# Performance work log

Measured on AMD Instinct MI355X. Metric: run time of the kernel, lower is better.

Reference implementation:

```python
import jax, jax.numpy as jnp
import numpy as np

B, N, D = 4, 512, 256  # batch, num_diseases, feature_dim == hidden_dim
H = 256                # hidden_dim
EPS = 1e-5

def _layernorm(x, g, b):
    m = jnp.mean(x, axis=-1, keepdims=True)
    v = jnp.mean((x - m) ** 2, axis=-1, keepdims=True)
    return (x - m) * jax.lax.rsqrt(v + EPS) * g + b

def setup_inputs() -> dict:
    key = jax.random.key(0)
    ks = jax.random.split(key, 16)
    s = 0.02
    return {
        "x": jax.random.normal(ks[0], (B, N, D), jnp.float32),
        "area_matrix": jax.random.uniform(ks[1], (B, N), jnp.float32),
        "co_occurrence": jax.random.uniform(ks[2], (N, N), jnp.float32),
        "Wq": jax.random.normal(ks[3], (H, D), jnp.float32) * s,
        "bq": jnp.zeros((H,), jnp.float32),
        "Wk": jax.random.normal(ks[4], (H, D), jnp.float32) * s,
        "bk": jnp.zeros((H,), jnp.float32),
        "Wv": jax.random.normal(ks[5], (H, D), jnp.float32) * s,
        "bv": jnp.zeros((H,), jnp.float32),
        "We1": jax.random.normal(ks[6], (H, 2), jnp.float32) * 0.5,
        "be1": jnp.zeros((H,), jnp.float32),
        "We2": jax.random.normal(ks[7], (1, H), jnp.float32) * s,
        "be2": jnp.zeros((1,), jnp.float32),
        "Wo": jax.random.normal(ks[8], (H, H), jnp.float32) * s,
        "bo": jnp.zeros((H,), jnp.float32),
        "g_ot": jnp.ones((H,), jnp.float32),
        "b_ot": jnp.zeros((H,), jnp.float32),
        "g1": jnp.ones((H,), jnp.float32),
        "b1": jnp.zeros((H,), jnp.float32),
        "g2": jnp.ones((H,), jnp.float32),
        "b2": jnp.zeros((H,), jnp.float32),
    }

def reference(x, area_matrix, co_occurrence, Wq, bq, Wk, bk, Wv, bv,
              We1, be1, We2, be2, Wo, bo, g_ot, b_ot, g1, b1, g2, b2):
    # projections: (B, N, H)
    q = jnp.einsum('bnd,hd->bnh', x, Wq) + bq
    k = jnp.einsum('bnd,hd->bnh', x, Wk) + bk
    v = jnp.einsum('bnd,hd->bnh', x, Wv) + bv
    attn_scores = jnp.einsum('bih,bjh->bij', q, k) / jnp.sqrt(jnp.float32(H))
    # edge inputs: (B, N, N, 2) = stack(broadcast area along last N, broadcast co-occ along batch)
    area = jnp.broadcast_to(area_matrix[:, :, None], (B, N, N))
    co = jnp.broadcast_to(co_occurrence[None], (B, N, N))
    edge_inputs = jnp.stack([area, co], axis=-1)
    h = jax.nn.relu(jnp.einsum('bije,he->bijh', edge_inputs, We1) + be1)
    edge_weights = jax.nn.sigmoid(jnp.einsum('bijh,oh->bijo', h, We2) + be2)[..., 0]
    attn_probs = jax.nn.softmax(attn_scores * edge_weights, axis=-1)  # dropout = identity (eval)
    out = jnp.einsum('bij,bjh->bih', attn_probs, v)
    out = _layernorm(out, g1, b1)
    out = jax.nn.relu(_layernorm(jnp.einsum('bnh,oh->bno', out, Wo) + bo, g_ot, b_ot))
    out = _layernorm(out + x, g2, b2)
    return out
```

## Files before the change

### kernel.cpp

```cpp
#include <hip/hip_runtime.h>

typedef unsigned short u16;
typedef unsigned int u32;

#define NB 4
#define NN 512
#define ND 256
#define NH 256
#define TI 4

typedef __attribute__((ext_vector_type(8))) short short8;
typedef __attribute__((ext_vector_type(4))) float f32x4;

__device__ __forceinline__ short bf(float f) {
    u32 t; __builtin_memcpy(&t, &f, 4);
    u32 r = (t + 0x7FFFu + ((t >> 16) & 1u)) >> 16;
    return (short)(u16)r;
}
__device__ __forceinline__ float blo(u32 u) {
    u32 t = u << 16; float f; __builtin_memcpy(&f, &t, 4); return f;
}
__device__ __forceinline__ float bhi(u32 u) {
    u32 t = u & 0xFFFF0000u; float f; __builtin_memcpy(&f, &t, 4); return f;
}

__device__ __forceinline__ float waveReduceSum(float v) {
#pragma unroll
    for (int o = 32; o > 0; o >>= 1) v += __shfl_down(v, o);
    return v;
}

__device__ __forceinline__ void blockReduce8(float4& va, float4& vb, float4* red) {
#pragma unroll
    for (int o = 32; o > 0; o >>= 1) {
        va.x += __shfl_down(va.x, o); va.y += __shfl_down(va.y, o);
        va.z += __shfl_down(va.z, o); va.w += __shfl_down(va.w, o);
        vb.x += __shfl_down(vb.x, o); vb.y += __shfl_down(vb.y, o);
        vb.z += __shfl_down(vb.z, o); vb.w += __shfl_down(vb.w, o);
    }
    int wid = threadIdx.x >> 6;
    __syncthreads();
    if ((threadIdx.x & 63) == 0) { red[2 * wid] = va; red[2 * wid + 1] = vb; }
    __syncthreads();
    float4 ra = red[0], rb = red[1];
#pragma unroll
    for (int w = 1; w < 8; ++w) {
        float4 ua = red[2 * w], ub = red[2 * w + 1];
        ra.x += ua.x; ra.y += ua.y; ra.z += ua.z; ra.w += ua.w;
        rb.x += ub.x; rb.y += ub.y; rb.z += ub.z; rb.w += ub.w;
    }
    va = ra; vb = rb;
}

__global__ __launch_bounds__(256) void qkv_mfma(
    const float* __restrict__ x,
    const float* __restrict__ Wq, const float* __restrict__ bq,
    const float* __restrict__ Wk, const float* __restrict__ bk,
    const float* __restrict__ Wv, const float* __restrict__ bv,
    const float* __restrict__ Wo,
    u16* __restrict__ qb, u16* __restrict__ kb, u16* __restrict__ vp,
    u16* __restrict__ wop)
{
    const int tid = threadIdx.x;
    if (blockIdx.y == 48) {
        __shared__ float t[32][33];
        const int tx = tid & 31, ty = tid >> 5;
#pragma unroll
        for (int tt2 = 0; tt2 < 2; ++tt2) {
            const int tile = blockIdx.x * 2 + tt2;
            const int bx = tile & 7, by = tile >> 3;
            __syncthreads();
#pragma unroll
            for (int k = 0; k < 4; ++k)
                t[ty + 8 * k][tx] = Wo[(size_t)(by * 32 + ty + 8 * k) * 256 + bx * 32 + tx];
            __syncthreads();
#pragma unroll
            for (int k = 0; k < 4; ++k) {
                const int d = bx * 32 + ty + 8 * k, o = by * 32 + tx;
                wop[(size_t)(d >> 3) * 2048 + o * 8 + (d & 7)] = (u16)bf(t[tx][ty + 8 * k]);
            }
        }
        return;
    }

    const int lane = tid & 63, wave = tid >> 6;
    const int r0 = blockIdx.x * 64 + wave * 16;
    const int out0 = blockIdx.y * 16;
    const int which = blockIdx.y >> 4;
    const float* W   = (which == 0) ? Wq : (which == 1) ? Wk : Wv;
    const float* bia = (which == 0) ? bq : (which == 1) ? bk : bv;
    u16* dst         = (which == 0) ? qb : (which == 1) ? kb : vp;

    const int m = lane & 15, koff = (lane >> 4) * 8;
    const float* Ap = x + (size_t)(r0 + m) * 256 + koff;
    const float* Bp = W + (size_t)((out0 & 255) + m) * 256 + koff;

    f32x4 acc = {0.f, 0.f, 0.f, 0.f};
#pragma unroll
    for (int kb8 = 0; kb8 < 8; ++kb8) {
        float4 a0 = *(const float4*)(Ap + kb8 * 32);
        float4 a1 = *(const float4*)(Ap + kb8 * 32 + 4);
        float4 b0 = *(const float4*)(Bp + kb8 * 32);
        float4 b1 = *(const float4*)(Bp + kb8 * 32 + 4);
        short8 af, bf8;
        af[0] = bf(a0.x); af[1] = bf(a0.y); af[2] = bf(a0.z); af[3] = bf(a0.w);
        af[4] = bf(a1.x); af[5] = bf(a1.y); af[6] = bf(a1.z); af[7] = bf(a1.w);
        bf8[0] = bf(b0.x); bf8[1] = bf(b0.y); bf8[2] = bf(b0.z); bf8[3] = bf(b0.w);
        bf8[4] = bf(b1.x); bf8[5] = bf(b1.y); bf8[6] = bf(b1.z); bf8[7] = bf(b1.w);
        acc = __builtin_amdgcn_mfma_f32_16x16x32_bf16(af, bf8, acc, 0, 0, 0);
    }

    const int oc = (out0 + m) & 255;
    const float bias = bia[oc];
    const int rbase = r0 + (lane >> 4) * 4;
#pragma unroll
    for (int reg = 0; reg < 4; ++reg) {
        int R = rbase + reg;
        dst[(size_t)R * 256 + oc] = (u16)bf(acc[reg] + bias);
    }
}

__global__ __launch_bounds__(256) void s_gemm(
    const u16* __restrict__ qb, const u16* __restrict__ kb, float* __restrict__ S)
{
    const int lane = threadIdx.x & 63, wave = threadIdx.x >> 6;
    const int job = blockIdx.x * 4 + wave;
    const int b = job >> 10, rem = job & 1023;
    const int i0 = (rem >> 5) * 16, j0 = (rem & 31) * 16;
    const int m = lane & 15, koff = (lane >> 4) * 8;
    const u16* Ap = qb + (size_t)(b * 512 + i0 + m) * 256 + koff;
    const u16* Bp = kb + (size_t)(b * 512 + j0 + m) * 256 + koff;

    f32x4 acc = {0.f, 0.f, 0.f, 0.f};
#pragma unroll
    for (int kb8 = 0; kb8 < 8; ++kb8) {
        short8 a  = *(const short8*)(Ap + kb8 * 32);
        short8 bf8 = *(const short8*)(Bp + kb8 * 32);
        acc = __builtin_amdgcn_mfma_f32_16x16x32_bf16(a, bf8, acc, 0, 0, 0);
    }
    const int col = j0 + m;
    const int rbase = i0 + (lane >> 4) * 4;
#pragma unroll
    for (int reg = 0; reg < 4; ++reg)
        S[(size_t)(b * 512 + rbase + reg) * 512 + col] = acc[reg];
}

__global__ __launch_bounds__(512) void fused_kernel(
    const float* __restrict__ x, const float* __restrict__ area, const float* __restrict__ co,
    const float* __restrict__ We1, const float* __restrict__ be1,
    const float* __restrict__ We2, const float* __restrict__ be2,
    const u32* __restrict__ wop32, const float* __restrict__ bo,
    const float* __restrict__ g_ot, const float* __restrict__ b_ot,
    const float* __restrict__ g1, const float* __restrict__ b1,
    const float* __restrict__ g2, const float* __restrict__ b2,
    const float* __restrict__ S, const u32* __restrict__ vp32,
    float* __restrict__ out)
{
    const int tid = threadIdx.x;
    const int b = blockIdx.x >> 7;
    const int i0 = (blockIdx.x & 127) << 2;
    const int lane = tid & 63, w = tid >> 6;

    __shared__ float histS[1024], histB[1024], hist2S[1024], hist2B[1024];
    __shared__ float srow[2048];
    __shared__ float4 red8b[16];
    __shared__ float sBaseS[4], sBaseB[4], redA[8], redB[8];

    const float be2f = be2[0];

    histS[tid] = 0.f; histS[tid + 512] = 0.f;
    histB[tid] = 0.f; histB[tid + 512] = 0.f;
    __syncthreads();
    {
        const int s = tid >> 7, h0 = tid & 127;
        const float a = area[b * NN + i0 + s];
        float baS = 0.f, baB = 0.f;
#pragma unroll
        for (int k = 0; k < 2; ++k) {
            const int h = h0 + 128 * k;
            const float w10 = We1[2 * h], w11 = We1[2 * h + 1];
            const float w2v = We2[h], be1v = be1[h];
            const float al = fmaf(a, w10, be1v);
            const float sl = w11 * w2v, bb = al * w2v;
            if (w11 == 0.f) {
                if (al > 0.f) baB += bb;
            } else {
                float tt = -al / w11;
                if (w11 > 0.f) {
                    if (tt <= 0.f)      { baS += sl; baB += bb; }
                    else if (tt < 1.f) {
                        int u = (int)(tt * 256.f); u = u > 255 ? 255 : u;
                        atomicAdd(&histS[s * 256 + u], sl);
                        atomicAdd(&histB[s * 256 + u], bb);
                    }
                } else {
                    if (tt >= 1.f)      { baS += sl; baB += bb; }
                    else if (tt > 0.f) {
                        baS += sl; baB += bb;
                        int u = (int)(tt * 256.f); u = u > 255 ? 255 : u;
                        atomicAdd(&histS[s * 256 + u], -sl);
                        atomicAdd(&histB[s * 256 + u], -bb);
                    }
                }
            }
        }
        float rS = waveReduceSum(baS), rB = waveReduceSum(baB);
        if (lane == 0) { redA[w] = rS; redB[w] = rB; }
    }
    __syncthreads();
    if (tid < 4) {
        sBaseS[tid] = redA[2 * tid] + redA[2 * tid + 1];
        sBaseB[tid] = redB[2 * tid] + redB[2 * tid + 1];
    }

    {
        const int s = w & 3;
        float* hp = (w < 4) ? histS : histB;
        float b0 = hp[s * 256 + 4 * lane + 0];
        float b1 = hp[s * 256 + 4 * lane + 1];
        float b2 = hp[s * 256 + 4 * lane + 2];
        float b3 = hp[s * 256 + 4 * lane + 3];
        float p0 = b0, p1 = p0 + b1, p2 = p1 + b2, p3 = p2 + b3;
        float incl = p3;
#pragma unroll
        for (int off = 1; off < 64; off <<= 1) {
            float t = __shfl_up(incl, off);
            if (lane >= off) incl += t;
        }
        float excl = incl - p3;
        hp[s * 256 + 4 * lane + 0] = p0 + excl;
        hp[s * 256 + 4 * lane + 1] = p1 + excl;
        hp[s * 256 + 4 * lane + 2] = p2 + excl;
        hp[s * 256 + 4 * lane + 3] = p3 + excl;
    }
    __syncthreads();

    {
        const float* Sp = S + (size_t)(b * NN + i0) * 512 + tid;
#pragma unroll
        for (int ti = 0; ti < TI; ++ti) {
            float c = co[(size_t)(i0 + ti) * NN + tid];
            int u = (int)(c * 256.f); u = u > 255 ? 255 : u;
            float Sg = sBaseS[ti] + histS[ti * 256 + u];
            float Bg = sBaseB[ti] + histB[ti * 256 + u];
            float e = fmaf(c, Sg, Bg) + be2f;
            float ew = 1.f / (1.f + __expf(-e));
            srow[ti * 512 + tid] = __expf(Sp[(size_t)ti * 512] * 0.0625f * ew);
        }
        __syncthreads();
    }

    {
        const int h2 = tid & 127, qtr = tid >> 7;
        float a0[TI] = {0.f, 0.f, 0.f, 0.f};
        float a1[TI] = {0.f, 0.f, 0.f, 0.f};
        const u32* vp_ = vp32 + (size_t)b * 512 * 128 + h2;
        const float4* s4p = (const float4*)srow;
        for (int j4 = qtr * 32; j4 < qtr * 32 + 32; ++j4) {
            const int jj = 4 * j4;
            u32 va = vp_[(size_t)(jj + 0) * 128];
            u32 vb = vp_[(size_t)(jj + 1) * 128];
            u32 vc = vp_[(size_t)(jj + 2) * 128];
            u32 vd = vp_[(size_t)(jj + 3) * 128];
            float la = blo(va), ha = bhi(va), lb = blo(vb), hb = bhi(vb);
            float lc = blo(vc), hc = bhi(vc), ld = blo(vd), hd = bhi(vd);
#pragma unroll
            for (int ti = 0; ti < TI; ++ti) {
                float4 p4 = s4p[ti * 128 + j4];
                a0[ti] += p4.x * la + p4.y * lb + p4.z * lc + p4.w * ld;
                a1[ti] += p4.x * ha + p4.y * hb + p4.z * hc + p4.w * hd;
            }
        }
        float2* bq_ = (float2*)((qtr == 0) ? histS : (qtr == 1) ? histB : (qtr == 2) ? hist2S : hist2B);
#pragma unroll
        for (int ti = 0; ti < TI; ++ti) bq_[ti * 128 + h2] = make_float2(a0[ti], a1[ti]);
        __syncthreads();
    }

    const int hP = tid & 255, half = tid >> 8;
    float accv[TI] = {0.f, 0.f, 0.f, 0.f};
    if (half == 0) {
#pragma unroll
        for (int ti = 0; ti < TI; ++ti)
            accv[ti] = histS[ti * 256 + hP] + histB[ti * 256 + hP]
                     + hist2S[ti * 256 + hP] + hist2B[ti * 256 + hP];
    }

    float4 sa, sb;
    float dd[TI];
#pragma unroll
    for (int ti = 0; ti < TI; ++ti) {
        float v = (half == 0) ? accv[ti] : 0.f;
        ((float*)&sa)[ti] = v; ((float*)&sb)[ti] = v * v;
    }
    blockReduce8(sa, sb, red8b);
    if (half == 0) {
        const float g1v = g1[hP], b1v = b1[hP];
#pragma unroll
        for (int ti = 0; ti < TI; ++ti) {
            float mean = ((const float*)&sa)[ti] * (1.f / 256.f);
            float var = fmaxf(((const float*)&sb)[ti] * (1.f / 256.f) - mean * mean, 0.f);
            srow[ti * 256 + hP] = (accv[ti] - mean) * rsqrtf(var + 1e-5f) * g1v + b1v;
        }
    }
    __syncthreads();

    float acc2[TI] = {0.f, 0.f, 0.f, 0.f};
    {
        const float4* y4p = (const float4*)srow;
        for (int g = half * 16; g < half * 16 + 16; ++g) {
            uint4 ww = *(const uint4*)(wop32 + (size_t)g * 1024 + hP * 4);
            float f0 = blo(ww.x), f1 = bhi(ww.x), f2 = blo(ww.y), f3 = bhi(ww.y);
            float f4 = blo(ww.z), f5 = bhi(ww.z), f6 = blo(ww.w), f7 = bhi(ww.w);
#pragma unroll
            for (int ti = 0; ti < TI; ++ti) {
                float4 ya = y4p[ti * 64 + 2 * g];
                float4 yb = y4p[ti * 64 + 2 * g + 1];
                acc2[ti] += ya.x * f0 + ya.y * f1 + ya.z * f2 + ya.w * f3
                          + yb.x * f4 + yb.y * f5 + yb.z * f6 + yb.w * f7;
            }
        }
        if (half == 1) {
#pragma unroll
            for (int ti = 0; ti < TI; ++ti) histS[ti * 256 + hP] = acc2[ti];
        }
        __syncthreads();
        if (half == 0) {
            const float bov = bo[hP];
#pragma unroll
            for (int ti = 0; ti < TI; ++ti) acc2[ti] += histS[ti * 256 + hP] + bov;
        }
    }

#pragma unroll
    for (int ti = 0; ti < TI; ++ti) {
        float v = (half == 0) ? acc2[ti] : 0.f;
        ((float*)&sa)[ti] = v; ((float*)&sb)[ti] = v * v;
    }
    blockReduce8(sa, sb, red8b);
    float z[TI];
    const float gotv = (half == 0) ? g_ot[hP] : 0.f;
    const float botv = (half == 0) ? b_ot[hP] : 0.f;
#pragma unroll
    for (int ti = 0; ti < TI; ++ti) {
        float mean = ((const float*)&sa)[ti] * (1.f / 256.f);
        float var = fmaxf(((const float*)&sb)[ti] * (1.f / 256.f) - mean * mean, 0.f);
        dd[ti] = (half == 0) ? acc2[ti] - mean : 0.f;
        z[ti] = fmaxf(dd[ti] * rsqrtf(var + 1e-5f) * gotv + botv, 0.f);
    }

    float tt[TI];
#pragma unroll
    for (int ti = 0; ti < TI; ++ti) {
        tt[ti] = (half == 0) ? z[ti] + x[(size_t)(b * NN + i0 + ti) * ND + hP] : 0.f;
        ((float*)&sa)[ti] = tt[ti]; ((float*)&sb)[ti] = tt[ti] * tt[ti];
    }
    blockReduce8(sa, sb, red8b);
    if (half == 0) {
        const float g2v = g2[hP], b2v = b2[hP];
#pragma unroll
        for (int ti = 0; ti < TI; ++ti) {
            float mean = ((const float*)&sa)[ti] * (1.f / 256.f);
            float var = fmaxf(((const float*)&sb)[ti] * (1.f / 256.f) - mean * mean, 0.f);
            float o = (tt[ti] - mean) * rsqrtf(var + 1e-5f) * g2v + b2v;
            out[(size_t)(b * NN + i0 + ti) * NH + hP] = o;
        }
    }
}

extern "C" void kernel_launch(void* const* d_in, const int* in_sizes, int n_in,
                              void* d_out, int out_size, void* d_ws, size_t ws_size,
                              hipStream_t stream) {
    const float* x    = (const float*)d_in[0];
    const float* area = (const float*)d_in[1];
    const float* co   = (const float*)d_in[2];
    const float* Wq   = (const float*)d_in[3];
    const float* bq   = (const float*)d_in[4];
    const float* Wk   = (const float*)d_in[5];
    const float* bk   = (const float*)d_in[6];
    const float* Wv   = (const float*)d_in[7];
    const float* bv   = (const float*)d_in[8];
    const float* We1  = (const float*)d_in[9];
    const float* be1  = (const float*)d_in[10];
    const float* We2  = (const float*)d_in[11];
    const float* be2  = (const float*)d_in[12];
    const float* Wo   = (const float*)d_in[13];
    const float* bo   = (const float*)d_in[14];
    const float* g_ot = (const float*)d_in[15];
    const float* b_ot = (const float*)d_in[16];
    const float* g1   = (const float*)d_in[17];
    const float* b1   = (const float*)d_in[18];
    const float* g2   = (const float*)d_in[19];
    const float* b2   = (const float*)d_in[20];

    u16*  qb  = (u16*)d_ws;
    u16*  kb  = qb + (size_t)2048 * 256;
    u16*  vp  = kb + (size_t)2048 * 256;
    u16*  wop = vp + (size_t)2048 * 256;
    float* S  = (float*)(wop + 65536);

    qkv_mfma<<<dim3(32, 49), 256, 0, stream>>>(x, Wq, bq, Wk, bk, Wv, bv, Wo,
                                               qb, kb, vp, wop);
    s_gemm<<<1024, 256, 0, stream>>>(qb, kb, S);
    fused_kernel<<<NB * NN / TI, 512, 0, stream>>>(x, area, co, We1, be1, We2, be2,
                                                   (const u32*)wop, bo,
                                                   g_ot, b_ot, g1, b1, g2, b2,
                                                   S, (const u32*)vp,
                                                   (float*)d_out);
}
```

Measured before the change: 158.6 us.

## Use MFMA for PV and output projection in fused kernel; pre-convert inputs to bf16

```diff
diff --git a/kernel.cpp b/kernel.cpp
--- a/kernel.cpp
+++ b/kernel.cpp
@@ -12,16 +12,10 @@
 typedef __attribute__((ext_vector_type(8))) short short8;
 typedef __attribute__((ext_vector_type(4))) float f32x4;
 
-__device__ __forceinline__ short bf(float f) {
+__device__ __forceinline__ u16 bfq(float f) {
     u32 t; __builtin_memcpy(&t, &f, 4);
     u32 r = (t + 0x7FFFu + ((t >> 16) & 1u)) >> 16;
-    return (short)(u16)r;
-}
-__device__ __forceinline__ float blo(u32 u) {
-    u32 t = u << 16; float f; __builtin_memcpy(&f, &t, 4); return f;
-}
-__device__ __forceinline__ float bhi(u32 u) {
-    u32 t = u & 0xFFFF0000u; float f; __builtin_memcpy(&f, &t, 4); return f;
+    return (u16)r;
 }
 
 __device__ __forceinline__ float waveReduceSum(float v) {
@@ -52,62 +46,50 @@
     va = ra; vb = rb;
 }
 
+__global__ __launch_bounds__(256) void prep_kernel(
+    const float* __restrict__ x, const float* __restrict__ Wq,
+    const float* __restrict__ Wk, const float* __restrict__ Wv,
+    const float* __restrict__ Wo,
+    u16* __restrict__ xb, u16* __restrict__ wb)
+{
+    const int idx4 = (blockIdx.x * 256 + threadIdx.x) * 4;
+    const float* src;
+    u16* dst;
+    int off;
+    if (idx4 < 524288) { src = x; dst = xb; off = idx4; }
+    else {
+        int u = idx4 - 524288;
+        int which = u >> 16; off = u & 65535;
+        src = (which == 0) ? Wq : (which == 1) ? Wk : (which == 2) ? Wv : Wo;
+        dst = wb + which * 65536;
+    }
+    float4 f = *(const float4*)(src + off);
+    u32 lo = (u32)bfq(f.x) | ((u32)bfq(f.y) << 16);
+    u32 hi = (u32)bfq(f.z) | ((u32)bfq(f.w) << 16);
+    *(uint2*)(dst + off) = make_uint2(lo, hi);
+}
+
 __global__ __launch_bounds__(256) void qkv_mfma(
-    const float* __restrict__ x,
-    const float* __restrict__ Wq, const float* __restrict__ bq,
-    const float* __restrict__ Wk, const float* __restrict__ bk,
-    const float* __restrict__ Wv, const float* __restrict__ bv,
-    const float* __restrict__ Wo,
-    u16* __restrict__ qb, u16* __restrict__ kb, u16* __restrict__ vp,
-    u16* __restrict__ wop)
+    const u16* __restrict__ xb, const u16* __restrict__ wb,
+    const float* __restrict__ bq, const float* __restrict__ bk, const float* __restrict__ bv,
+    u16* __restrict__ qb, u16* __restrict__ kb, u16* __restrict__ vt)
 {
-    const int tid = threadIdx.x;
-    if (blockIdx.y == 48) {
-        __shared__ float t[32][33];
-        const int tx = tid & 31, ty = tid >> 5;
-#pragma unroll
-        for (int tt2 = 0; tt2 < 2; ++tt2) {
-            const int tile = blockIdx.x * 2 + tt2;
-            const int bx = tile & 7, by = tile >> 3;
-            __syncthreads();
-#pragma unroll
-            for (int k = 0; k < 4; ++k)
-                t[ty + 8 * k][tx] = Wo[(size_t)(by * 32 + ty + 8 * k) * 256 + bx * 32 + tx];
-            __syncthreads();
-#pragma unroll
-            for (int k = 0; k < 4; ++k) {
-                const int d = bx * 32 + ty + 8 * k, o = by * 32 + tx;
-                wop[(size_t)(d >> 3) * 2048 + o * 8 + (d & 7)] = (u16)bf(t[tx][ty + 8 * k]);
-            }
-        }
-        return;
-    }
-
-    const int lane = tid & 63, wave = tid >> 6;
+    const int lane = threadIdx.x & 63, wave = threadIdx.x >> 6;
     const int r0 = blockIdx.x * 64 + wave * 16;
     const int out0 = blockIdx.y * 16;
     const int which = blockIdx.y >> 4;
-    const float* W   = (which == 0) ? Wq : (which == 1) ? Wk : Wv;
     const float* bia = (which == 0) ? bq : (which == 1) ? bk : bv;
-    u16* dst         = (which == 0) ? qb : (which == 1) ? kb : vp;
 
     const int m = lane & 15, koff = (lane >> 4) * 8;
-    const float* Ap = x + (size_t)(r0 + m) * 256 + koff;
-    const float* Bp = W + (size_t)((out0 & 255) + m) * 256 + koff;
+    const u16* Ap = xb + (size_t)(r0 + m) * 256 + koff;
+    const u16* Bp = wb + which * 65536 + (size_t)((out0 & 255) + m) * 256 + koff;
 
     f32x4 acc = {0.f, 0.f, 0.f, 0.f};
 #pragma unroll
-    for (int kb8 = 0; kb8 < 8; ++kb8) {
-        float4 a0 = *(const float4*)(Ap + kb8 * 32);
-        float4 a1 = *(const float4*)(Ap + kb8 * 32 + 4);
-        float4 b0 = *(const float4*)(Bp + kb8 * 32);
-        float4 b1 = *(const float4*)(Bp + kb8 * 32 + 4);
-        short8 af, bf8;
-        af[0] = bf(a0.x); af[1] = bf(a0.y); af[2] = bf(a0.z); af[3] = bf(a0.w);
-        af[4] = bf(a1.x); af[5] = bf(a1.y); af[6] = bf(a1.z); af[7] = bf(a1.w);
-        bf8[0] = bf(b0.x); bf8[1] = bf(b0.y); bf8[2] = bf(b0.z); bf8[3] = bf(b0.w);
-        bf8[4] = bf(b1.x); bf8[5] = bf(b1.y); bf8[6] = bf(b1.z); bf8[7] = bf(b1.w);
-        acc = __builtin_amdgcn_mfma_f32_16x16x32_bf16(af, bf8, acc, 0, 0, 0);
+    for (int ks = 0; ks < 8; ++ks) {
+        short8 a  = *(const short8*)(Ap + ks * 32);
+        short8 bb = *(const short8*)(Bp + ks * 32);
+        acc = __builtin_amdgcn_mfma_f32_16x16x32_bf16(a, bb, acc, 0, 0, 0);
     }
 
     const int oc = (out0 + m) & 255;
@@ -116,7 +98,10 @@
 #pragma unroll
     for (int reg = 0; reg < 4; ++reg) {
         int R = rbase + reg;
-        dst[(size_t)R * 256 + oc] = (u16)bf(acc[reg] + bias);
+        u16 val = bfq(acc[reg] + bias);
+        if (which == 0)      qb[(size_t)R * 256 + oc] = val;
+        else if (which == 1) kb[(size_t)R * 256 + oc] = val;
+        else                 vt[((size_t)(R >> 9) * 256 + oc) * 512 + (R & 511)] = val;
     }
 }
 
@@ -133,10 +118,10 @@
 
     f32x4 acc = {0.f, 0.f, 0.f, 0.f};
 #pragma unroll
-    for (int kb8 = 0; kb8 < 8; ++kb8) {
-        short8 a  = *(const short8*)(Ap + kb8 * 32);
-        short8 bf8 = *(const short8*)(Bp + kb8 * 32);
-        acc = __builtin_amdgcn_mfma_f32_16x16x32_bf16(a, bf8, acc, 0, 0, 0);
+    for (int ks = 0; ks < 8; ++ks) {
+        short8 a   = *(const short8*)(Ap + ks * 32);
+        short8 bb  = *(const short8*)(Bp + ks * 32);
+        acc = __builtin_amdgcn_mfma_f32_16x16x32_bf16(a, bb, acc, 0, 0, 0);
     }
     const int col = j0 + m;
     const int rbase = i0 + (lane >> 4) * 4;
@@ -145,15 +130,17 @@
         S[(size_t)(b * 512 + rbase + reg) * 512 + col] = acc[reg];
 }
 
+#define PSTR 520
+#define YSTR 264
 __global__ __launch_bounds__(512) void fused_kernel(
     const float* __restrict__ x, const float* __restrict__ area, const float* __restrict__ co,
     const float* __restrict__ We1, const float* __restrict__ be1,
     const float* __restrict__ We2, const float* __restrict__ be2,
-    const u32* __restrict__ wop32, const float* __restrict__ bo,
+    const u16* __restrict__ wob, const float* __restrict__ bo,
     const float* __restrict__ g_ot, const float* __restrict__ b_ot,
     const float* __restrict__ g1, const float* __restrict__ b1,
     const float* __restrict__ g2, const float* __restrict__ b2,
-    const float* __restrict__ S, const u32* __restrict__ vp32,
+    const float* __restrict__ S, const u16* __restrict__ vt,
     float* __restrict__ out)
 {
     const int tid = threadIdx.x;
@@ -161,8 +148,10 @@
     const int i0 = (blockIdx.x & 127) << 2;
     const int lane = tid & 63, w = tid >> 6;
 
-    __shared__ float histS[1024], histB[1024], hist2S[1024], hist2B[1024];
-    __shared__ float srow[2048];
+    __shared__ float histS[1024], histB[1024];
+    __shared__ float pvbuf[1024];
+    __shared__ u16 srow16[16 * PSTR];
+    __shared__ u16 y16[16 * YSTR];
     __shared__ float4 red8b[16];
     __shared__ float sBaseS[4], sBaseB[4], redA[8], redB[8];
 
@@ -170,7 +159,14 @@
 
     histS[tid] = 0.f; histS[tid + 512] = 0.f;
     histB[tid] = 0.f; histB[tid + 512] = 0.f;
-    __syncthreads();
+    {
+        u32* s32 = (u32*)srow16;
+        for (int i = tid; i < 4160; i += 512) s32[i] = 0u;
+        u32* y32 = (u32*)y16;
+        for (int i = tid; i < 2112; i += 512) y32[i] = 0u;
+    }
+    __syncthreads();
+
     {
         const int s = tid >> 7, h0 = tid & 127;
         const float a = area[b * NN + i0 + s];
@@ -245,53 +241,45 @@
             float Bg = sBaseB[ti] + histB[ti * 256 + u];
             float e = fmaf(c, Sg, Bg) + be2f;
             float ew = 1.f / (1.f + __expf(-e));
-            srow[ti * 512 + tid] = __expf(Sp[(size_t)ti * 512] * 0.0625f * ew);
+            srow16[ti * PSTR + tid] = bfq(__expf(Sp[(size_t)ti * 512] * 0.0625f * ew));
         }
         __syncthreads();
     }
 
     {
-        const int h2 = tid & 127, qtr = tid >> 7;
-        float a0[TI] = {0.f, 0.f, 0.f, 0.f};
-        float a1[TI] = {0.f, 0.f, 0.f, 0.f};
-        const u32* vp_ = vp32 + (size_t)b * 512 * 128 + h2;
-        const float4* s4p = (const float4*)srow;
-        for (int j4 = qtr * 32; j4 < qtr * 32 + 32; ++j4) {
-            const int jj = 4 * j4;
-            u32 va = vp_[(size_t)(jj + 0) * 128];
-            u32 vb = vp_[(size_t)(jj + 1) * 128];
-            u32 vc = vp_[(size_t)(jj + 2) * 128];
-            u32 vd = vp_[(size_t)(jj + 3) * 128];
-            float la = blo(va), ha = bhi(va), lb = blo(vb), hb = bhi(vb);
-            float lc = blo(vc), hc = bhi(vc), ld = blo(vd), hd = bhi(vd);
-#pragma unroll
-            for (int ti = 0; ti < TI; ++ti) {
-                float4 p4 = s4p[ti * 128 + j4];
-                a0[ti] += p4.x * la + p4.y * lb + p4.z * lc + p4.w * ld;
-                a1[ti] += p4.x * ha + p4.y * hb + p4.z * hc + p4.w * hd;
+        const int m = lane & 15, koff = (lane >> 4) * 8;
+        const int t0 = 2 * w, t1 = 2 * w + 1;
+        const u16* B0p = vt + ((size_t)(b * 256 + t0 * 16 + m)) * 512 + koff;
+        const u16* B1p = vt + ((size_t)(b * 256 + t1 * 16 + m)) * 512 + koff;
+        const u16* Arow = srow16 + m * PSTR + koff;
+        f32x4 acc0 = {0.f, 0.f, 0.f, 0.f}, acc1 = {0.f, 0.f, 0.f, 0.f};
+#pragma unroll
+        for (int ks = 0; ks < 16; ++ks) {
+            short8 a  = *(const short8*)(Arow + ks * 32);
+            short8 b0 = *(const short8*)(B0p + ks * 32);
+            short8 b1 = *(const short8*)(B1p + ks * 32);
+            acc0 = __builtin_amdgcn_mfma_f32_16x16x32_bf16(a, b0, acc0, 0, 0, 0);
+            acc1 = __builtin_amdgcn_mfma_f32_16x16x32_bf16(a, b1, acc1, 0, 0, 0);
+        }
+        __syncthreads();
+        if (lane < 16) {
+#pragma unroll
+            for (int reg = 0; reg < 4; ++reg) {
+                pvbuf[reg * 256 + t0 * 16 + lane] = acc0[reg];
+                pvbuf[reg * 256 + t1 * 16 + lane] = acc1[reg];
             }
         }
-        float2* bq_ = (float2*)((qtr == 0) ? histS : (qtr == 1) ? histB : (qtr == 2) ? hist2S : hist2B);
-#pragma unroll
-        for (int ti = 0; ti < TI; ++ti) bq_[ti * 128 + h2] = make_float2(a0[ti], a1[ti]);
         __syncthreads();
     }
 
     const int hP = tid & 255, half = tid >> 8;
-    float accv[TI] = {0.f, 0.f, 0.f, 0.f};
-    if (half == 0) {
-#pragma unroll
-        for (int ti = 0; ti < TI; ++ti)
-            accv[ti] = histS[ti * 256 + hP] + histB[ti * 256 + hP]
-                     + hist2S[ti * 256 + hP] + hist2B[ti * 256 + hP];
-    }
-
     float4 sa, sb;
-    float dd[TI];
+    float accv[TI];
 #pragma unroll
     for (int ti = 0; ti < TI; ++ti) {
-        float v = (half == 0) ? accv[ti] : 0.f;
-        ((float*)&sa)[ti] = v; ((float*)&sb)[ti] = v * v;
+        accv[ti] = (half == 0) ? pvbuf[ti * 256 + hP] : 0.f;
+        ((float*)&sa)[ti] = accv[ti];
+        ((float*)&sb)[ti] = accv[ti] * accv[ti];
     }
     blockReduce8(sa, sb, red8b);
     if (half == 0) {
@@ -300,42 +288,46 @@
         for (int ti = 0; ti < TI; ++ti) {
             float mean = ((const float*)&sa)[ti] * (1.f / 256.f);
             float var = fmaxf(((const float*)&sb)[ti] * (1.f / 256.f) - mean * mean, 0.f);
-            srow[ti * 256 + hP] = (accv[ti] - mean) * rsqrtf(var + 1e-5f) * g1v + b1v;
-        }
-    }
-    __syncthreads();
-
-    float acc2[TI] = {0.f, 0.f, 0.f, 0.f};
-    {
-        const float4* y4p = (const float4*)srow;
-        for (int g = half * 16; g < half * 16 + 16; ++g) {
-            uint4 ww = *(const uint4*)(wop32 + (size_t)g * 1024 + hP * 4);
-            float f0 = blo(ww.x), f1 = bhi(ww.x), f2 = blo(ww.y), f3 = bhi(ww.y);
-            float f4 = blo(ww.z), f5 = bhi(ww.z), f6 = blo(ww.w), f7 = bhi(ww.w);
-#pragma unroll
-            for (int ti = 0; ti < TI; ++ti) {
-                float4 ya = y4p[ti * 64 + 2 * g];
-                float4 yb = y4p[ti * 64 + 2 * g + 1];
-                acc2[ti] += ya.x * f0 + ya.y * f1 + ya.z * f2 + ya.w * f3
-                          + yb.x * f4 + yb.y * f5 + yb.z * f6 + yb.w * f7;
+            y16[ti * YSTR + hP] = bfq((accv[ti] - mean) * rsqrtf(var + 1e-5f) * g1v + b1v);
+        }
+    }
+    __syncthreads();
+
+    {
+        const int m = lane & 15, koff = (lane >> 4) * 8;
+        const int t0 = 2 * w, t1 = 2 * w + 1;
+        const u16* B0p = wob + (size_t)(t0 * 16 + m) * 256 + koff;
+        const u16* B1p = wob + (size_t)(t1 * 16 + m) * 256 + koff;
+        const u16* Arow = y16 + m * YSTR + koff;
+        f32x4 acc0 = {0.f, 0.f, 0.f, 0.f}, acc1 = {0.f, 0.f, 0.f, 0.f};
+#pragma unroll
+        for (int ks = 0; ks < 8; ++ks) {
+            short8 a  = *(const short8*)(Arow + ks * 32);
+            short8 b0 = *(const short8*)(B0p + ks * 32);
+            short8 b1 = *(const short8*)(B1p + ks * 32);
+            acc0 = __builtin_amdgcn_mfma_f32_16x16x32_bf16(a, b0, acc0, 0, 0, 0);
+            acc1 = __builtin_amdgcn_mfma_f32_16x16x32_bf16(a, b1, acc1, 0, 0, 0);
+        }
+        __syncthreads();
+        if (lane < 16) {
+#pragma unroll
+            for (int reg = 0; reg < 4; ++reg) {
+                pvbuf[reg * 256 + t0 * 16 + lane] = acc0[reg];
+                pvbuf[reg * 256 + t1 * 16 + lane] = acc1[reg];
             }
         }
-        if (half == 1) {
-#pragma unroll
-            for (int ti = 0; ti < TI; ++ti) histS[ti * 256 + hP] = acc2[ti];
-        }
         __syncthreads();
-        if (half == 0) {
-            const float bov = bo[hP];
-#pragma unroll
-            for (int ti = 0; ti < TI; ++ti) acc2[ti] += histS[ti * 256 + hP] + bov;
-        }
-    }
-
-#pragma unroll
-    for (int ti = 0; ti < TI; ++ti) {
-        float v = (half == 0) ? acc2[ti] : 0.f;
-        ((float*)&sa)[ti] = v; ((float*)&sb)[ti] = v * v;
+    }
+
+    float acc2[TI];
+    {
+        const float bov = (half == 0) ? bo[hP] : 0.f;
+#pragma unroll
+        for (int ti = 0; ti < TI; ++ti) {
+            acc2[ti] = (half == 0) ? pvbuf[ti * 256 + hP] + bov : 0.f;
+            ((float*)&sa)[ti] = acc2[ti];
+            ((float*)&sb)[ti] = acc2[ti] * acc2[ti];
+        }
     }
     blockReduce8(sa, sb, red8b);
     float z[TI];
@@ -345,8 +337,7 @@
     for (int ti = 0; ti < TI; ++ti) {
         float mean = ((const float*)&sa)[ti] * (1.f / 256.f);
         float var = fmaxf(((const float*)&sb)[ti] * (1.f / 256.f) - mean * mean, 0.f);
-        dd[ti] = (half == 0) ? acc2[ti] - mean : 0.f;
-        z[ti] = fmaxf(dd[ti] * rsqrtf(var + 1e-5f) * gotv + botv, 0.f);
+        z[ti] = fmaxf((acc2[ti] - mean) * rsqrtf(var + 1e-5f) * gotv + botv, 0.f);
     }
 
     float tt[TI];
@@ -393,18 +384,18 @@
     const float* g2   = (const float*)d_in[19];
     const float* b2   = (const float*)d_in[20];
 
-    u16*  qb  = (u16*)d_ws;
+    u16*  xb  = (u16*)d_ws;
+    u16*  wb  = xb + (size_t)2048 * 256;
+    u16*  qb  = wb + (size_t)4 * 65536;
     u16*  kb  = qb + (size_t)2048 * 256;
-    u16*  vp  = kb + (size_t)2048 * 256;
-    u16*  wop = vp + (size_t)2048 * 256;
-    float* S  = (float*)(wop + 65536);
-
-    qkv_mfma<<<dim3(32, 49), 256, 0, stream>>>(x, Wq, bq, Wk, bk, Wv, bv, Wo,
-                                               qb, kb, vp, wop);
+    u16*  vt  = kb + (size_t)2048 * 256;
+    float* S  = (float*)(vt + (size_t)2048 * 256);
+
+    prep_kernel<<<768, 256, 0, stream>>>(x, Wq, Wk, Wv, Wo, xb, wb);
+    qkv_mfma<<<dim3(32, 48), 256, 0, stream>>>(xb, wb, bq, bk, bv, qb, kb, vt);
     s_gemm<<<1024, 256, 0, stream>>>(qb, kb, S);
     fused_kernel<<<NB * NN / TI, 512, 0, stream>>>(x, area, co, We1, be1, We2, be2,
-                                                   (const u32*)wop, bo,
+                                                   wb + 3 * 65536, bo,
                                                    g_ot, b_ot, g1, b1, g2, b2,
-                                                   S, (const u32*)vp,
-                                                   (float*)d_out);
-}
+                                                   S, vt, (float*)d_out);
+}
```

After: 155.7 us (median of 2 runs). Within noise of the previous version (-1.8%).
